# Optimization experiments

Measured on AMD Instinct MI355X. Metric: run time of the kernel, lower is better.

The kernel has to match this reference:

```python
import jax, jax.numpy as jnp
import numpy as np

N_NODES = 500000
N_EDGES = 2000000
F_IN = 117
HIDDEN = 128
NLAYERS = 3


def setup_inputs() -> dict:
    key = jax.random.key(0)
    ks = jax.random.split(key, 8)
    x = jax.random.normal(ks[0], (N_NODES, F_IN), dtype=jnp.float32)
    edge_src = jax.random.randint(ks[1], (N_EDGES,), 0, N_NODES, dtype=jnp.int32)
    edge_dst = jax.random.randint(ks[2], (N_EDGES,), 0, N_NODES, dtype=jnp.int32)
    W_in = jax.random.normal(ks[3], (F_IN, HIDDEN), dtype=jnp.float32) * 0.05
    b_in = jax.random.normal(ks[4], (HIDDEN,), dtype=jnp.float32) * 0.05
    W_self = jax.random.normal(ks[5], (NLAYERS, HIDDEN, HIDDEN), dtype=jnp.float32) * 0.05
    W_neigh = jax.random.normal(ks[6], (NLAYERS, HIDDEN, HIDDEN), dtype=jnp.float32) * 0.05
    b_layers = jax.random.normal(ks[7], (NLAYERS, HIDDEN), dtype=jnp.float32) * 0.05
    return {"x": x, "edge_src": edge_src, "edge_dst": edge_dst,
            "W_in": W_in, "b_in": b_in,
            "W_self": W_self, "W_neigh": W_neigh, "b_layers": b_layers}


def reference(x, edge_src, edge_dst, W_in, b_in, W_self, W_neigh, b_layers):
    # Input projection: Linear(117 -> 128) + Tanh
    h = jnp.tanh(x @ W_in + b_in)  # [N, H]
    N = h.shape[0]

    # In-degree per destination node (static; zero-degree nodes get zero mean)
    deg = jax.ops.segment_sum(jnp.ones_like(edge_dst, dtype=h.dtype), edge_dst,
                              num_segments=N)  # [N]
    inv_deg = (1.0 / jnp.maximum(deg, 1.0))[:, None]  # [N, 1]

    # Stacked SAGEConv('mean') layers: relu(h @ W_self + mean_neigh @ W_neigh + b)
    for l in range(NLAYERS):
        neigh_sum = jax.ops.segment_sum(h[edge_src], edge_dst, num_segments=N)  # [N, H]
        h_neigh = neigh_sum * inv_deg
        h = jax.nn.relu(h @ W_self[l] + h_neigh @ W_neigh[l] + b_layers[l])
    return h
```

## Files before the change

kernel.cpp:

```cpp
#include <hip/hip_runtime.h>

#define N_NODES 500000
#define N_EDGES 2000000
#define F_IN 117
#define H 128
#define NLAYERS 3

#define SCAN_E 2048
#define NB_SCAN ((N_NODES + SCAN_E - 1) / SCAN_E)

typedef __attribute__((ext_vector_type(8))) short short8v;
typedef __attribute__((ext_vector_type(4))) float f32x4;

__device__ __forceinline__ unsigned short f2bf(float x) {
    unsigned u = __builtin_bit_cast(unsigned, x);
    u += 0x7FFFu + ((u >> 16) & 1u);
    return (unsigned short)(u >> 16);
}
__device__ __forceinline__ float bf2f(unsigned short s) {
    unsigned u = ((unsigned)s) << 16;
    return __builtin_bit_cast(float, u);
}
__device__ __forceinline__ float fast_tanh(float x) {
    float e = __builtin_amdgcn_exp2f(x * 2.885390081777927f);
    return 1.0f - 2.0f * __builtin_amdgcn_rcpf(e + 1.0f);
}

__global__ void prep_w_kernel(const float* __restrict__ Wself,
                              const float* __restrict__ Wneigh,
                              const float* __restrict__ Win,
                              short* __restrict__ Wfrag,
                              short* __restrict__ WfragIn) {
    const int tid = blockIdx.x * 256 + threadIdx.x;
    const int total_cmb = NLAYERS * 64 * 64;
    if (tid < total_cmb) {
        const int lane = tid & 63;
        const int fi   = (tid >> 6) & 63;
        const int l    = tid >> 12;
        const int ks = fi & 7, ct = (fi >> 3) & 3, wc = fi >> 5;
        const int c = wc * 64 + ct * 16 + (lane & 15);
        const int kbase = ks * 32 + (lane >> 4) * 8;
        short8v out;
        #pragma unroll
        for (int j = 0; j < 8; ++j) {
            int k = kbase + j;
            float v = (k < 128) ? Wself [(size_t)l * H * H + k * H + c]
                                : Wneigh[(size_t)l * H * H + (k - 128) * H + c];
            out[j] = (short)f2bf(v);
        }
        *(short8v*)(Wfrag + (size_t)tid * 8) = out;
    } else if (tid < total_cmb + 32 * 64) {
        const int t2 = tid - total_cmb;
        const int lane = t2 & 63;
        const int fi   = t2 >> 6;
        const int ks = fi & 3, ct = (fi >> 2) & 3, wc = fi >> 4;
        const int c = wc * 64 + ct * 16 + (lane & 15);
        const int kbase = ks * 32 + (lane >> 4) * 8;
        short8v out;
        #pragma unroll
        for (int j = 0; j < 8; ++j) {
            int k = kbase + j;
            out[j] = (k < F_IN) ? (short)f2bf(Win[(size_t)k * H + c]) : (short)0;
        }
        *(short8v*)(WfragIn + (size_t)t2 * 8) = out;
    }
}

__global__ __launch_bounds__(512, 2) void proj_mfma(const short* __restrict__ WfragIn,
                                                    const float* __restrict__ bias,
                                                    const float* __restrict__ x,
                                                    unsigned short* __restrict__ hb) {
    const int wave = threadIdx.x >> 6;
    const int lane = threadIdx.x & 63;
    const int wc   = wave & 1;

    short8v Bf[4][4];
    #pragma unroll
    for (int ct = 0; ct < 4; ++ct)
        #pragma unroll
        for (int ks = 0; ks < 4; ++ks)
            Bf[ct][ks] = ((const short8v*)WfragIn)[(size_t)(((wc * 4 + ct) * 4 + ks) * 64 + lane)];

    float bs[4];
    #pragma unroll
    for (int ct = 0; ct < 4; ++ct) bs[ct] = bias[wc * 64 + ct * 16 + (lane & 15)];

    const int cbase = (lane >> 4) * 8;
    const int ntasks = (N_NODES / 16) * 2;
    for (int task = blockIdx.x * 8 + wave; task < ntasks; task += gridDim.x * 8) {
        const int r0  = (task >> 1) * 16;
        const int row = r0 + (lane & 15);
        const float* xr = x + (size_t)row * F_IN;

        short8v Af[4];
        #pragma unroll
        for (int ks = 0; ks < 4; ++ks) {
            const int k0 = ks * 32 + cbase;
            short8v a;
            if (row == N_NODES - 1 && k0 + 7 >= F_IN) {
                #pragma unroll
                for (int j = 0; j < 8; ++j) {
                    int k = k0 + j;
                    a[j] = (k < F_IN) ? (short)f2bf(xr[k]) : (short)0;
                }
            } else {
                #pragma unroll
                for (int j = 0; j < 8; ++j) a[j] = (short)f2bf(xr[k0 + j]);
            }
            Af[ks] = a;
        }

        f32x4 acc[4];
        #pragma unroll
        for (int ct = 0; ct < 4; ++ct) acc[ct] = (f32x4){0.f, 0.f, 0.f, 0.f};
        #pragma unroll
        for (int ks = 0; ks < 4; ++ks)
            #pragma unroll
            for (int ct = 0; ct < 4; ++ct)
                acc[ct] = __builtin_amdgcn_mfma_f32_16x16x32_bf16(Af[ks], Bf[ct][ks], acc[ct], 0, 0, 0);

        #pragma unroll
        for (int ct = 0; ct < 4; ++ct) {
            const int col = wc * 64 + ct * 16 + (lane & 15);
            #pragma unroll
            for (int q = 0; q < 4; ++q) {
                float v = fast_tanh(acc[ct][q] + bs[ct]);
                hb[(size_t)(r0 + (lane >> 4) * 4 + q) * H + col] = f2bf(v);
            }
        }
    }
}

__global__ void zero_int_kernel(int* __restrict__ p, int n) {
    int i = blockIdx.x * blockDim.x + threadIdx.x;
    if (i < n) p[i] = 0;
}

__global__ void hist_kernel(const int* __restrict__ dst, int* __restrict__ cnt) {
    int e = blockIdx.x * blockDim.x + threadIdx.x;
    if (e < N_EDGES) atomicAdd(&cnt[dst[e]], 1);
}

__global__ __launch_bounds__(256) void scan_reduce_kernel(const int* __restrict__ cnt,
                                                          int* __restrict__ bsums) {
    __shared__ int s[256];
    const int base = blockIdx.x * SCAN_E;
    int sum = 0;
    for (int i = threadIdx.x; i < SCAN_E; i += 256) {
        int idx = base + i;
        sum += (idx < N_NODES) ? cnt[idx] : 0;
    }
    s[threadIdx.x] = sum;
    __syncthreads();
    for (int off = 128; off > 0; off >>= 1) {
        if (threadIdx.x < off) s[threadIdx.x] += s[threadIdx.x + off];
        __syncthreads();
    }
    if (threadIdx.x == 0) bsums[blockIdx.x] = s[0];
}

__global__ void scan_bsums_kernel(int* __restrict__ bsums) {
    __shared__ int s[256];
    const int tid = threadIdx.x;
    int v = (tid < NB_SCAN) ? bsums[tid] : 0;
    s[tid] = v;
    __syncthreads();
    for (int off = 1; off < 256; off <<= 1) {
        int add = (tid >= off) ? s[tid - off] : 0;
        __syncthreads();
        s[tid] += add;
        __syncthreads();
    }
    if (tid < NB_SCAN) bsums[tid] = s[tid] - v;
}

__global__ __launch_bounds__(256) void scan_final_kernel(const int* __restrict__ cnt,
                                                         const int* __restrict__ bsums,
                                                         int* __restrict__ start,
                                                         int* __restrict__ cursor,
                                                         float* __restrict__ inv) {
    __shared__ int tsum[256];
    const int tid = threadIdx.x;
    const int base = blockIdx.x * SCAN_E + tid * 8;
    int c[8];
    int s = 0;
    #pragma unroll
    for (int k = 0; k < 8; ++k) {
        int idx = base + k;
        c[k] = (idx < N_NODES) ? cnt[idx] : 0;
        s += c[k];
    }
    tsum[tid] = s;
    __syncthreads();
    for (int off = 1; off < 256; off <<= 1) {
        int add = (tid >= off) ? tsum[tid - off] : 0;
        __syncthreads();
        tsum[tid] += add;
        __syncthreads();
    }
    int off0 = bsums[blockIdx.x] + tsum[tid] - s;
    #pragma unroll
    for (int k = 0; k < 8; ++k) {
        int idx = base + k;
        if (idx < N_NODES) {
            start[idx]  = off0;
            cursor[idx] = off0;
            inv[idx]    = 1.0f / fmaxf((float)c[k], 1.0f);
            off0 += c[k];
        }
    }
}

__global__ void fill_kernel(const int* __restrict__ src, const int* __restrict__ dst,
                            int* __restrict__ cursor, int* __restrict__ srcs) {
    int e = blockIdx.x * blockDim.x + threadIdx.x;
    if (e < N_EDGES) {
        int pos = atomicAdd(&cursor[dst[e]], 1);
        srcs[pos] = src[e];
    }
}

__global__ __launch_bounds__(256) void gather_kernel(const int* __restrict__ start,
                                                     const int* __restrict__ cnt,
                                                     const int* __restrict__ srcs,
                                                     const float* __restrict__ inv,
                                                     const unsigned short* __restrict__ hb,
                                                     unsigned short* __restrict__ nsb) {
    const int idx  = blockIdx.x * 256 + threadIdx.x;
    const int node = idx >> 4;
    if (node >= N_NODES) return;
    const int f = (idx & 15) * 8;
    const int st = start[node];
    const int c  = cnt[node];
    float a[8];
    #pragma unroll
    for (int i = 0; i < 8; ++i) a[i] = 0.f;
    int j = 0;
    for (; j + 4 <= c; j += 4) {
        const int s0 = srcs[st + j + 0];
        const int s1 = srcs[st + j + 1];
        const int s2 = srcs[st + j + 2];
        const int s3 = srcs[st + j + 3];
        const short8v v0 = *(const short8v*)(hb + (size_t)s0 * H + f);
        const short8v v1 = *(const short8v*)(hb + (size_t)s1 * H + f);
        const short8v v2 = *(const short8v*)(hb + (size_t)s2 * H + f);
        const short8v v3 = *(const short8v*)(hb + (size_t)s3 * H + f);
        #pragma unroll
        for (int i = 0; i < 8; ++i)
            a[i] += (bf2f((unsigned short)v0[i]) + bf2f((unsigned short)v1[i]))
                  + (bf2f((unsigned short)v2[i]) + bf2f((unsigned short)v3[i]));
    }
    if (j + 2 <= c) {
        const int s0 = srcs[st + j + 0];
        const int s1 = srcs[st + j + 1];
        const short8v v0 = *(const short8v*)(hb + (size_t)s0 * H + f);
        const short8v v1 = *(const short8v*)(hb + (size_t)s1 * H + f);
        #pragma unroll
        for (int i = 0; i < 8; ++i)
            a[i] += bf2f((unsigned short)v0[i]) + bf2f((unsigned short)v1[i]);
        j += 2;
    }
    if (j < c) {
        const int s0 = srcs[st + j];
        const short8v v0 = *(const short8v*)(hb + (size_t)s0 * H + f);
        #pragma unroll
        for (int i = 0; i < 8; ++i) a[i] += bf2f((unsigned short)v0[i]);
    }
    const float iv = inv[node];
    short8v o;
    #pragma unroll
    for (int i = 0; i < 8; ++i) o[i] = (short)f2bf(a[i] * iv);
    *(short8v*)(nsb + (size_t)node * H + f) = o;
}

__global__ __launch_bounds__(512, 2) void combine_mfma(const short* __restrict__ Wfrag,
                                                       const float* __restrict__ bias,
                                                       const unsigned short* __restrict__ hb,
                                                       const unsigned short* __restrict__ nsb,
                                                       unsigned short* __restrict__ outb,
                                                       float* __restrict__ outf,
                                                       int last) {
    const int wave = threadIdx.x >> 6;
    const int lane = threadIdx.x & 63;
    const int wc   = wave & 1;

    short8v Bf[4][8];
    #pragma unroll
    for (int ct = 0; ct < 4; ++ct)
        #pragma unroll
        for (int ks = 0; ks < 8; ++ks)
            Bf[ct][ks] = ((const short8v*)Wfrag)[(size_t)(((wc * 4 + ct) * 8 + ks) * 64 + lane)];

    float bs[4];
    #pragma unroll
    for (int ct = 0; ct < 4; ++ct) bs[ct] = bias[wc * 64 + ct * 16 + (lane & 15)];

    const int ntasks = (N_NODES / 16) * 2;
    for (int task = blockIdx.x * 8 + wave; task < ntasks; task += gridDim.x * 8) {
        const int r0 = (task >> 1) * 16;
        const unsigned short* arow = hb  + (size_t)(r0 + (lane & 15)) * H + (lane >> 4) * 8;
        const unsigned short* nrow = nsb + (size_t)(r0 + (lane & 15)) * H + (lane >> 4) * 8;
        short8v Af[8];
        #pragma unroll
        for (int ks = 0; ks < 4; ++ks) Af[ks]     = *(const short8v*)(arow + ks * 32);
        #pragma unroll
        for (int ks = 0; ks < 4; ++ks) Af[4 + ks] = *(const short8v*)(nrow + ks * 32);

        f32x4 acc[4];
        #pragma unroll
        for (int ct = 0; ct < 4; ++ct) acc[ct] = (f32x4){0.f, 0.f, 0.f, 0.f};
        #pragma unroll
        for (int ks = 0; ks < 8; ++ks)
            #pragma unroll
            for (int ct = 0; ct < 4; ++ct)
                acc[ct] = __builtin_amdgcn_mfma_f32_16x16x32_bf16(Af[ks], Bf[ct][ks], acc[ct], 0, 0, 0);

        if (!last) {
            #pragma unroll
            for (int ct = 0; ct < 4; ++ct) {
                const int col = wc * 64 + ct * 16 + (lane & 15);
                #pragma unroll
                for (int q = 0; q < 4; ++q) {
                    float v = fmaxf(acc[ct][q] + bs[ct], 0.f);
                    outb[(size_t)(r0 + (lane >> 4) * 4 + q) * H + col] = f2bf(v);
                }
            }
        } else {
            #pragma unroll
            for (int ct = 0; ct < 4; ++ct) {
                const int col = wc * 64 + ct * 16 + (lane & 15);
                #pragma unroll
                for (int q = 0; q < 4; ++q) {
                    float v = fmaxf(acc[ct][q] + bs[ct], 0.f);
                    outf[(size_t)(r0 + (lane >> 4) * 4 + q) * H + col] = v;
                }
            }
        }
    }
}

extern "C" void kernel_launch(void* const* d_in, const int* in_sizes, int n_in,
                              void* d_out, int out_size, void* d_ws, size_t ws_size,
                              hipStream_t stream) {
    const float* x        = (const float*)d_in[0];
    const int*   edge_src = (const int*)d_in[1];
    const int*   edge_dst = (const int*)d_in[2];
    const float* W_in     = (const float*)d_in[3];
    const float* b_in     = (const float*)d_in[4];
    const float* W_self   = (const float*)d_in[5];
    const float* W_neigh  = (const float*)d_in[6];
    const float* b_layers = (const float*)d_in[7];

    unsigned short* h0  = (unsigned short*)d_ws;
    unsigned short* nsb = h0 + (size_t)N_NODES * H;
    int*   cnt    = (int*)(nsb + (size_t)N_NODES * H);
    int*   start  = cnt + N_NODES;
    int*   cursor = start + N_NODES;
    float* inv    = (float*)(cursor + N_NODES);
    int*   srcs   = (int*)(inv + N_NODES);
    int*   bsums  = srcs + N_EDGES;
    short* Wfrag  = (short*)(bsums + 256);
    short* WfragIn = Wfrag + (size_t)NLAYERS * 64 * 64 * 8;
    unsigned short* h1 = (unsigned short*)d_out;

    prep_w_kernel<<<(NLAYERS * 64 * 64 + 32 * 64 + 255) / 256, 256, 0, stream>>>(
        W_self, W_neigh, W_in, Wfrag, WfragIn);

    zero_int_kernel<<<(N_NODES + 255) / 256, 256, 0, stream>>>(cnt, N_NODES);
    hist_kernel<<<(N_EDGES + 255) / 256, 256, 0, stream>>>(edge_dst, cnt);
    scan_reduce_kernel<<<NB_SCAN, 256, 0, stream>>>(cnt, bsums);
    scan_bsums_kernel<<<1, 256, 0, stream>>>(bsums);
    scan_final_kernel<<<NB_SCAN, 256, 0, stream>>>(cnt, bsums, start, cursor, inv);
    fill_kernel<<<(N_EDGES + 255) / 256, 256, 0, stream>>>(edge_src, edge_dst, cursor, srcs);

    proj_mfma<<<1024, 512, 0, stream>>>(WfragIn, b_in, x, h0);

    const int gather_grid = (N_NODES * 16 + 255) / 256;
    gather_kernel<<<gather_grid, 256, 0, stream>>>(start, cnt, srcs, inv, h0, nsb);
    combine_mfma<<<1024, 512, 0, stream>>>(Wfrag + 0 * 64 * 64 * 8, b_layers + 0 * H,
                                           h0, nsb, h1, nullptr, 0);
    gather_kernel<<<gather_grid, 256, 0, stream>>>(start, cnt, srcs, inv, h1, nsb);
    combine_mfma<<<1024, 512, 0, stream>>>(Wfrag + 1 * 64 * 64 * 8, b_layers + 1 * H,
                                           h1, nsb, h0, nullptr, 0);
    gather_kernel<<<gather_grid, 256, 0, stream>>>(start, cnt, srcs, inv, h0, nsb);
    combine_mfma<<<1024, 512, 0, stream>>>(Wfrag + 2 * 64 * 64 * 8, b_layers + 2 * H,
                                           h0, nsb, nullptr, (float*)d_out, 1);
}
```

Measured before the change: 1.031 ms.

## Fuse neighbor mean gather into MFMA combine kernel per layer

Removes the separate gather kernel and the intermediate neighbor-mean buffer. Each wave now gathers and averages neighbor features for its 16 rows directly into registers, then feeds them as the second half of the MFMA K dimension. This saves the write and re-read of the nsb array and three kernel launches. In exchange, each lane walks a whole node's edge list serially with 32 float accumulators. The combine kernel's occupancy limit (512 threads, 2 blocks) now also governs the latency-bound gather, and the same rows are gathered redundantly by both column-half waves.

```diff
diff --git a/kernel.cpp b/kernel.cpp
--- a/kernel.cpp
+++ b/kernel.cpp
@@ -220,66 +220,16 @@
     }
 }
 
-__global__ __launch_bounds__(256) void gather_kernel(const int* __restrict__ start,
-                                                     const int* __restrict__ cnt,
-                                                     const int* __restrict__ srcs,
-                                                     const float* __restrict__ inv,
-                                                     const unsigned short* __restrict__ hb,
-                                                     unsigned short* __restrict__ nsb) {
-    const int idx  = blockIdx.x * 256 + threadIdx.x;
-    const int node = idx >> 4;
-    if (node >= N_NODES) return;
-    const int f = (idx & 15) * 8;
-    const int st = start[node];
-    const int c  = cnt[node];
-    float a[8];
-    #pragma unroll
-    for (int i = 0; i < 8; ++i) a[i] = 0.f;
-    int j = 0;
-    for (; j + 4 <= c; j += 4) {
-        const int s0 = srcs[st + j + 0];
-        const int s1 = srcs[st + j + 1];
-        const int s2 = srcs[st + j + 2];
-        const int s3 = srcs[st + j + 3];
-        const short8v v0 = *(const short8v*)(hb + (size_t)s0 * H + f);
-        const short8v v1 = *(const short8v*)(hb + (size_t)s1 * H + f);
-        const short8v v2 = *(const short8v*)(hb + (size_t)s2 * H + f);
-        const short8v v3 = *(const short8v*)(hb + (size_t)s3 * H + f);
-        #pragma unroll
-        for (int i = 0; i < 8; ++i)
-            a[i] += (bf2f((unsigned short)v0[i]) + bf2f((unsigned short)v1[i]))
-                  + (bf2f((unsigned short)v2[i]) + bf2f((unsigned short)v3[i]));
-    }
-    if (j + 2 <= c) {
-        const int s0 = srcs[st + j + 0];
-        const int s1 = srcs[st + j + 1];
-        const short8v v0 = *(const short8v*)(hb + (size_t)s0 * H + f);
-        const short8v v1 = *(const short8v*)(hb + (size_t)s1 * H + f);
-        #pragma unroll
-        for (int i = 0; i < 8; ++i)
-            a[i] += bf2f((unsigned short)v0[i]) + bf2f((unsigned short)v1[i]);
-        j += 2;
-    }
-    if (j < c) {
-        const int s0 = srcs[st + j];
-        const short8v v0 = *(const short8v*)(hb + (size_t)s0 * H + f);
-        #pragma unroll
-        for (int i = 0; i < 8; ++i) a[i] += bf2f((unsigned short)v0[i]);
-    }
-    const float iv = inv[node];
-    short8v o;
-    #pragma unroll
-    for (int i = 0; i < 8; ++i) o[i] = (short)f2bf(a[i] * iv);
-    *(short8v*)(nsb + (size_t)node * H + f) = o;
-}
-
-__global__ __launch_bounds__(512, 2) void combine_mfma(const short* __restrict__ Wfrag,
-                                                       const float* __restrict__ bias,
-                                                       const unsigned short* __restrict__ hb,
-                                                       const unsigned short* __restrict__ nsb,
-                                                       unsigned short* __restrict__ outb,
-                                                       float* __restrict__ outf,
-                                                       int last) {
+__global__ __launch_bounds__(512, 2) void fused_combine(const short* __restrict__ Wfrag,
+                                                        const float* __restrict__ bias,
+                                                        const int* __restrict__ start,
+                                                        const int* __restrict__ cnt,
+                                                        const int* __restrict__ srcs,
+                                                        const float* __restrict__ inv,
+                                                        const unsigned short* __restrict__ hb,
+                                                        unsigned short* __restrict__ outb,
+                                                        float* __restrict__ outf,
+                                                        int last) {
     const int wave = threadIdx.x >> 6;
     const int lane = threadIdx.x & 63;
     const int wc   = wave & 1;
@@ -295,25 +245,62 @@
     #pragma unroll
     for (int ct = 0; ct < 4; ++ct) bs[ct] = bias[wc * 64 + ct * 16 + (lane & 15)];
 
+    const int cbase = (lane >> 4) * 8;
     const int ntasks = (N_NODES / 16) * 2;
     for (int task = blockIdx.x * 8 + wave; task < ntasks; task += gridDim.x * 8) {
-        const int r0 = (task >> 1) * 16;
-        const unsigned short* arow = hb  + (size_t)(r0 + (lane & 15)) * H + (lane >> 4) * 8;
-        const unsigned short* nrow = nsb + (size_t)(r0 + (lane & 15)) * H + (lane >> 4) * 8;
-        short8v Af[8];
-        #pragma unroll
-        for (int ks = 0; ks < 4; ++ks) Af[ks]     = *(const short8v*)(arow + ks * 32);
-        #pragma unroll
-        for (int ks = 0; ks < 4; ++ks) Af[4 + ks] = *(const short8v*)(nrow + ks * 32);
+        const int r0  = (task >> 1) * 16;
+        const int row = r0 + (lane & 15);
+
+        const unsigned short* arow = hb + (size_t)row * H + cbase;
+        short8v Af[4];
+        #pragma unroll
+        for (int ks = 0; ks < 4; ++ks) Af[ks] = *(const short8v*)(arow + ks * 32);
+
+        float na[4][8];
+        #pragma unroll
+        for (int ks = 0; ks < 4; ++ks)
+            #pragma unroll
+            for (int i = 0; i < 8; ++i) na[ks][i] = 0.f;
+
+        const int st = start[row];
+        const int c  = cnt[row];
+        for (int j = 0; j < c; ++j) {
+            const unsigned short* nb = hb + (size_t)srcs[st + j] * H + cbase;
+            const short8v v0 = *(const short8v*)(nb + 0);
+            const short8v v1 = *(const short8v*)(nb + 32);
+            const short8v v2 = *(const short8v*)(nb + 64);
+            const short8v v3 = *(const short8v*)(nb + 96);
+            #pragma unroll
+            for (int i = 0; i < 8; ++i) {
+                na[0][i] += bf2f((unsigned short)v0[i]);
+                na[1][i] += bf2f((unsigned short)v1[i]);
+                na[2][i] += bf2f((unsigned short)v2[i]);
+                na[3][i] += bf2f((unsigned short)v3[i]);
+            }
+        }
+        const float iv = inv[row];
+        short8v An[4];
+        #pragma unroll
+        for (int ks = 0; ks < 4; ++ks) {
+            short8v a;
+            #pragma unroll
+            for (int i = 0; i < 8; ++i) a[i] = (short)f2bf(na[ks][i] * iv);
+            An[ks] = a;
+        }
 
         f32x4 acc[4];
         #pragma unroll
         for (int ct = 0; ct < 4; ++ct) acc[ct] = (f32x4){0.f, 0.f, 0.f, 0.f};
         #pragma unroll
-        for (int ks = 0; ks < 8; ++ks)
+        for (int ks = 0; ks < 4; ++ks)
             #pragma unroll
             for (int ct = 0; ct < 4; ++ct)
                 acc[ct] = __builtin_amdgcn_mfma_f32_16x16x32_bf16(Af[ks], Bf[ct][ks], acc[ct], 0, 0, 0);
+        #pragma unroll
+        for (int ks = 0; ks < 4; ++ks)
+            #pragma unroll
+            for (int ct = 0; ct < 4; ++ct)
+                acc[ct] = __builtin_amdgcn_mfma_f32_16x16x32_bf16(An[ks], Bf[ct][4 + ks], acc[ct], 0, 0, 0);
 
         if (!last) {
             #pragma unroll
@@ -375,14 +362,10 @@
 
     proj_mfma<<<1024, 512, 0, stream>>>(WfragIn, b_in, x, h0);
 
-    const int gather_grid = (N_NODES * 16 + 255) / 256;
-    gather_kernel<<<gather_grid, 256, 0, stream>>>(start, cnt, srcs, inv, h0, nsb);
-    combine_mfma<<<1024, 512, 0, stream>>>(Wfrag + 0 * 64 * 64 * 8, b_layers + 0 * H,
-                                           h0, nsb, h1, nullptr, 0);
-    gather_kernel<<<gather_grid, 256, 0, stream>>>(start, cnt, srcs, inv, h1, nsb);
-    combine_mfma<<<1024, 512, 0, stream>>>(Wfrag + 1 * 64 * 64 * 8, b_layers + 1 * H,
-                                           h1, nsb, h0, nullptr, 0);
-    gather_kernel<<<gather_grid, 256, 0, stream>>>(start, cnt, srcs, inv, h0, nsb);
-    combine_mfma<<<1024, 512, 0, stream>>>(Wfrag + 2 * 64 * 64 * 8, b_layers + 2 * H,
-                                           h0, nsb, nullptr, (float*)d_out, 1);
-}
+    fused_combine<<<1024, 512, 0, stream>>>(Wfrag + 0 * 64 * 64 * 8, b_layers + 0 * H,
+                                            start, cnt, srcs, inv, h0, h1, nullptr, 0);
+    fused_combine<<<1024, 512, 0, stream>>>(Wfrag + 1 * 64 * 64 * 8, b_layers + 1 * H,
+                                            start, cnt, srcs, inv, h1, h0, nullptr, 0);
+    fused_combine<<<1024, 512, 0, stream>>>(Wfrag + 2 * 64 * 64 * 8, b_layers + 2 * H,
+                                            start, cnt, srcs, inv, h0, nullptr, (float*)d_out, 1);
+}
```

After: 1.273 ms. 23.5% more time.

## Two-pass bucketed CSR fill to localize scattered atomics and writes

Applied to the files above, without the earlier changes.

Replaces the single-pass CSR fill, which does random per-node atomics and scattered writes, with two passes. The first bins (src,dst) pairs into 512-node buckets using bucket cursors. The second runs one block per bucket, placing the sources into final CSR positions with atomics that stay inside a small range. The aim is better cache locality for the atomics and writes. The cost is an extra kernel and another read and write of the edge pairs, which are staged in the nsb buffer.

```diff
diff --git a/kernel.cpp b/kernel.cpp
--- a/kernel.cpp
+++ b/kernel.cpp
@@ -8,6 +8,7 @@
 
 #define SCAN_E 2048
 #define NB_SCAN ((N_NODES + SCAN_E - 1) / SCAN_E)
+#define NBUCKET ((N_NODES + 511) >> 9)
 
 typedef __attribute__((ext_vector_type(8))) short short8v;
 typedef __attribute__((ext_vector_type(4))) float f32x4;
@@ -178,7 +179,8 @@
                                                          const int* __restrict__ bsums,
                                                          int* __restrict__ start,
                                                          int* __restrict__ cursor,
-                                                         float* __restrict__ inv) {
+                                                         float* __restrict__ inv,
+                                                         int* __restrict__ bcur) {
     __shared__ int tsum[256];
     const int tid = threadIdx.x;
     const int base = blockIdx.x * SCAN_E + tid * 8;
@@ -206,17 +208,34 @@
             start[idx]  = off0;
             cursor[idx] = off0;
             inv[idx]    = 1.0f / fmaxf((float)c[k], 1.0f);
+            if ((idx & 511) == 0) bcur[idx >> 9] = off0;
             off0 += c[k];
         }
     }
 }
 
-__global__ void fill_kernel(const int* __restrict__ src, const int* __restrict__ dst,
-                            int* __restrict__ cursor, int* __restrict__ srcs) {
+__global__ void bin_fill_kernel(const int* __restrict__ src, const int* __restrict__ dst,
+                                int* __restrict__ bcur, int2* __restrict__ pairs) {
     int e = blockIdx.x * blockDim.x + threadIdx.x;
     if (e < N_EDGES) {
-        int pos = atomicAdd(&cursor[dst[e]], 1);
-        srcs[pos] = src[e];
+        int d = dst[e];
+        int pos = atomicAdd(&bcur[d >> 9], 1);
+        pairs[pos] = make_int2(src[e], d);
+    }
+}
+
+__global__ __launch_bounds__(256) void bucket_scatter_kernel(const int* __restrict__ start,
+                                                             int* __restrict__ cursor,
+                                                             const int2* __restrict__ pairs,
+                                                             int* __restrict__ srcs) {
+    const int b = blockIdx.x;
+    const int ebeg = start[b << 9];
+    const int nn = (b + 1) << 9;
+    const int eend = (nn < N_NODES) ? start[nn] : N_EDGES;
+    for (int i = ebeg + threadIdx.x; i < eend; i += 256) {
+        int2 p = pairs[i];
+        int pos = atomicAdd(&cursor[p.y], 1);
+        srcs[pos] = p.x;
     }
 }
 
@@ -361,6 +380,8 @@
     int*   bsums  = srcs + N_EDGES;
     short* Wfrag  = (short*)(bsums + 256);
     short* WfragIn = Wfrag + (size_t)NLAYERS * 64 * 64 * 8;
+    int*   bcur   = (int*)(WfragIn + 32 * 64 * 8);
+    int2*  pairs  = (int2*)nsb;
     unsigned short* h1 = (unsigned short*)d_out;
 
     prep_w_kernel<<<(NLAYERS * 64 * 64 + 32 * 64 + 255) / 256, 256, 0, stream>>>(
@@ -370,8 +391,9 @@
     hist_kernel<<<(N_EDGES + 255) / 256, 256, 0, stream>>>(edge_dst, cnt);
     scan_reduce_kernel<<<NB_SCAN, 256, 0, stream>>>(cnt, bsums);
     scan_bsums_kernel<<<1, 256, 0, stream>>>(bsums);
-    scan_final_kernel<<<NB_SCAN, 256, 0, stream>>>(cnt, bsums, start, cursor, inv);
-    fill_kernel<<<(N_EDGES + 255) / 256, 256, 0, stream>>>(edge_src, edge_dst, cursor, srcs);
+    scan_final_kernel<<<NB_SCAN, 256, 0, stream>>>(cnt, bsums, start, cursor, inv, bcur);
+    bin_fill_kernel<<<(N_EDGES + 255) / 256, 256, 0, stream>>>(edge_src, edge_dst, bcur, pairs);
+    bucket_scatter_kernel<<<NBUCKET, 256, 0, stream>>>(start, cursor, pairs, srcs);
 
     proj_mfma<<<1024, 512, 0, stream>>>(WfragIn, b_in, x, h0);
 
```

Measured after the change: 1.326 ms. 28.6% more time.
